# Kernel optimization log

Measured on AMD Instinct MI355X. Metric: run time of the kernel, lower is better.

The kernel has to match this reference:

```python
import jax, jax.numpy as jnp
import numpy as np

ATT = 256  # att_fc_size
MIN_W = 32  # min_width_feat
EPS = 1e-5  # InstanceNorm eps


def setup_inputs() -> dict:
    key = jax.random.key(0)
    ks = jax.random.split(key, 16)
    B, C, H, W = 32, 256, 128, 256
    hid = 256
    s = 0.02
    inp = {
        'features': jax.random.normal(ks[0], (B, C, H, W), jnp.float32),
        'prev_attn_weights': jax.random.uniform(ks[1], (B, H), jnp.float32),
        'coverage_vector': jax.random.uniform(ks[2], (B, H), jnp.float32) * 2.0,
        'hidden_h': jax.random.normal(ks[3], (1, B, hid), jnp.float32),
        # dense_width: Linear(min_width, 1)
        'w_width': jax.random.normal(ks[4], (MIN_W, 1), jnp.float32) * s,
        'b_width': jnp.zeros((1,), jnp.float32),
        # dense_enc: Linear(C, att)
        'w_enc': jax.random.normal(ks[5], (C, ATT), jnp.float32) * s,
        'b_enc': jnp.zeros((ATT,), jnp.float32),
        # conv_block: Conv1d(2, 16, k=15, pad=7)  (OIW layout)
        'conv_w': jax.random.normal(ks[6], (16, 2, 15), jnp.float32) * s,
        'conv_b': jnp.zeros((16,), jnp.float32),
        # dense_conv_block: Linear(16, att)
        'w_cb': jax.random.normal(ks[7], (16, ATT), jnp.float32) * s,
        'b_cb': jnp.zeros((ATT,), jnp.float32),
        # dense_hidden: Linear(hidden, att)
        'w_hid': jax.random.normal(ks[8], (hid, ATT), jnp.float32) * s,
        'b_hid': jnp.zeros((ATT,), jnp.float32),
        # dense_align: Linear(att, 1)
        'w_align': jax.random.normal(ks[9], (ATT, 1), jnp.float32) * s,
        'b_align': jnp.zeros((1,), jnp.float32),
    }
    return inp


def reference(features, prev_attn_weights, coverage_vector, hidden_h,
              w_width, b_width, w_enc, b_enc, conv_w, conv_b,
              w_cb, b_cb, w_hid, b_hid, w_align, b_align):
    B, C, H, W = features.shape
    # AdaptiveMaxPool2d((None, MIN_W)) with W % MIN_W == 0 -> uniform window max
    hf = features.reshape(B, C, H, MIN_W, W // MIN_W).max(axis=-1)  # (B,C,H,MIN_W)
    # dense_width -> (B,C,H)
    h_features = (jnp.einsum('bchm,mo->bcho', hf, w_width) + b_width)[..., 0]
    # branch 1: dense_enc on (B,H,C)
    s = jnp.einsum('bhc,ca->bha', h_features.transpose(0, 2, 1), w_enc) + b_enc
    # location + coverage channels: (B,2,H)
    cat = jnp.stack([prev_attn_weights, jnp.clip(coverage_vector, 0.0, 1.0)], axis=1)
    # InstanceNorm1d (no affine): per (b, channel) over H
    mu = cat.mean(axis=-1, keepdims=True)
    var = cat.var(axis=-1, keepdims=True)
    cat = (cat - mu) * jax.lax.rsqrt(var + EPS)
    # Conv1d(2 -> 16, k=15, pad=7)
    conv = jax.lax.conv_general_dilated(
        cat, conv_w, window_strides=(1,), padding=[(7, 7)],
        dimension_numbers=('NCH', 'OIH', 'NCH')) + conv_b[None, :, None]  # (B,16,H)
    s = s + jnp.einsum('bhk,ka->bha', conv.transpose(0, 2, 1), w_cb) + b_cb
    # hidden branch: (1,B,hid) -> (1,B,att) -> (B,1,att), broadcasts over H
    hsum = (jnp.einsum('lbd,da->lba', hidden_h, w_hid) + b_hid).transpose(1, 0, 2)
    s = s + hsum
    s = jnp.tanh(s)
    align_score = jnp.einsum('bha,ao->bho', s, w_align) + b_align  # (B,H,1)
    attn = jax.nn.softmax(align_score, axis=1)  # softmax over H
    # context: features^T(H<->W) @ attn -> (B,C,W)
    context = jnp.einsum('bchw,bh->bcw', features, attn[..., 0])
    return context, attn[..., 0]
```

## Files before the change

### kernel.cpp

```cpp
#include <hip/hip_runtime.h>
#include <hip/hip_bf16.h>

#define B_DIM 32
#define C_DIM 256
#define H_DIM 128
#define W_DIM 256
#define ATT_DIM 256

__global__ __launch_bounds__(256) void ka_fused(
    const float* __restrict__ feat, const float* __restrict__ w_width,
    const float* __restrict__ b_width,
    const float* __restrict__ prev, const float* __restrict__ cov,
    const float* __restrict__ conv_w, const float* __restrict__ conv_b,
    const float* __restrict__ hidden, const float* __restrict__ w_hid,
    const float* __restrict__ b_hid, const float* __restrict__ b_enc,
    const float* __restrict__ b_cb,
    float* __restrict__ hf, float* __restrict__ convT, float* __restrict__ hsum)
{
  const int tid = threadIdx.x;
  const int bid = blockIdx.x;

  if (bid < 8192) {
    __shared__ float res[H_DIM];
    const int lane = tid & 63, wid = tid >> 6;
    const float wv = w_width[lane >> 1] * 0.5f;
    const float bw = b_width[0];
    const float* base = feat + (size_t)bid * H_DIM * W_DIM + lane * 4;
#pragma unroll 4
    for (int i = 0; i < 32; i++) {
      const int h = wid + 4 * i;
      float4 v4 = *reinterpret_cast<const float4*>(base + (size_t)h * W_DIM);
      float v = fmaxf(fmaxf(v4.x, v4.y), fmaxf(v4.z, v4.w));
      v = fmaxf(v, __shfl_xor(v, 1));
      float contrib = v * wv;
#pragma unroll
      for (int off = 32; off >= 1; off >>= 1) contrib += __shfl_xor(contrib, off);
      if (lane == 0) res[h] = contrib + bw;
    }
    __syncthreads();
    if (tid < H_DIM)
      hf[(size_t)bid * H_DIM + tid] = res[tid];
  } else if (bid < 8224) {
    const int b = bid - 8192;
    __shared__ float n0[H_DIM], n1[H_DIM];
    __shared__ float ws4[2][4];
    __shared__ float cw[480];
    for (int i = tid; i < 480; i += 256) cw[i] = conv_w[i];
    const int lane = tid & 63, wv2 = tid >> 6;
    float x0 = 0.f, x1 = 0.f;
    if (tid < 128) {
      x0 = prev[b * H_DIM + tid];
      x1 = cov[b * H_DIM + tid];
      x1 = fminf(fmaxf(x1, 0.0f), 1.0f);
      float s0 = x0, q0 = x0 * x0, s1 = x1, q1 = x1 * x1;
#pragma unroll
      for (int off = 32; off >= 1; off >>= 1) {
        s0 += __shfl_xor(s0, off); q0 += __shfl_xor(q0, off);
        s1 += __shfl_xor(s1, off); q1 += __shfl_xor(q1, off);
      }
      if (lane == 0) { ws4[wv2][0] = s0; ws4[wv2][1] = q0; ws4[wv2][2] = s1; ws4[wv2][3] = q1; }
    }
    __syncthreads();
    if (tid < 128) {
      float S0 = ws4[0][0] + ws4[1][0], Q0 = ws4[0][1] + ws4[1][1];
      float S1 = ws4[0][2] + ws4[1][2], Q1 = ws4[0][3] + ws4[1][3];
      const float rH = 1.0f / H_DIM;
      float mu0 = S0 * rH, mu1 = S1 * rH;
      float inv0 = 1.0f / sqrtf(Q0 * rH - mu0 * mu0 + 1e-5f);
      float inv1 = 1.0f / sqrtf(Q1 * rH - mu1 * mu1 + 1e-5f);
      n0[tid] = (x0 - mu0) * inv0;
      n1[tid] = (x1 - mu1) * inv1;
    }
    __syncthreads();
    if (tid < 128) {
      float o[16];
#pragma unroll
      for (int k = 0; k < 16; k++) o[k] = conv_b[k];
#pragma unroll
      for (int j = 0; j < 15; j++) {
        int hh = tid - 7 + j;
        if (hh >= 0 && hh < H_DIM) {
          float f0 = n0[hh], f1 = n1[hh];
#pragma unroll
          for (int k = 0; k < 16; k++)
            o[k] += f0 * cw[k * 30 + j] + f1 * cw[k * 30 + 15 + j];
        }
      }
      float* outp = convT + ((size_t)(b * H_DIM + tid)) * 16;
#pragma unroll
      for (int k = 0; k < 16; k++) outp[k] = o[k];
    }
  } else {
    const int b = bid - 8224;
    const int a = tid;
    float acc = b_hid[a] + b_enc[a] + b_cb[a];
    const float* hb = hidden + b * 256;
#pragma unroll 4
    for (int d = 0; d < 256; d++) acc += hb[d] * w_hid[d * ATT_DIM + a];
    hsum[b * ATT_DIM + a] = acc;
  }
}

__global__ __launch_bounds__(256) void kb_gemm_align(
    const float* __restrict__ hf, const float* __restrict__ convT,
    const float* __restrict__ hsum, const float* __restrict__ w_enc,
    const float* __restrict__ w_cb, const float* __restrict__ w_align,
    const float* __restrict__ b_align, float* __restrict__ align_out)
{
  __shared__ float At[C_DIM][12];
  __shared__ float Ct[16][9];
  __shared__ float red[8][ATT_DIM];
  const int tid = threadIdx.x;
  const int m0 = blockIdx.x * 8;
  const int b = m0 >> 7;
  const int h0 = m0 & 127;
  const float* hp = hf + ((size_t)(b * C_DIM + tid)) * H_DIM + h0;
  float4 r0 = *reinterpret_cast<const float4*>(hp);
  float4 r1 = *reinterpret_cast<const float4*>(hp + 4);
  *reinterpret_cast<float4*>(&At[tid][0]) = r0;
  *reinterpret_cast<float4*>(&At[tid][4]) = r1;
  if (tid < 128) {
    int m = tid >> 4, k = tid & 15;
    Ct[k][m] = convT[(size_t)(b * H_DIM + h0) * 16 + tid];
  }
  __syncthreads();
  float acc[8];
#pragma unroll
  for (int m = 0; m < 8; m++) acc[m] = 0.0f;
  const float* wep = w_enc + tid;
#pragma unroll 4
  for (int k = 0; k < C_DIM; k++) {
    float bv = wep[k * ATT_DIM];
    const float4 a0 = *reinterpret_cast<const float4*>(&At[k][0]);
    const float4 a1 = *reinterpret_cast<const float4*>(&At[k][4]);
    acc[0] += a0.x * bv; acc[1] += a0.y * bv; acc[2] += a0.z * bv; acc[3] += a0.w * bv;
    acc[4] += a1.x * bv; acc[5] += a1.y * bv; acc[6] += a1.z * bv; acc[7] += a1.w * bv;
  }
#pragma unroll
  for (int k = 0; k < 16; k++) {
    float bv = w_cb[k * ATT_DIM + tid];
#pragma unroll
    for (int m = 0; m < 8; m++) acc[m] += Ct[k][m] * bv;
  }
  const float hs = hsum[b * ATT_DIM + tid];
  const float wa = w_align[tid];
#pragma unroll
  for (int m = 0; m < 8; m++)
    red[m][tid] = tanhf(acc[m] + hs) * wa;
  __syncthreads();
  const int lane = tid & 63, wid = tid >> 6;
  const float ba = b_align[0];
  for (int m = wid; m < 8; m += 4) {
    float s = red[m][lane] + red[m][lane + 64] + red[m][lane + 128] + red[m][lane + 192];
#pragma unroll
    for (int off = 32; off >= 1; off >>= 1) s += __shfl_xor(s, off);
    if (lane == 0) align_out[m0 + m] = s + ba;
  }
}

__global__ __launch_bounds__(256) void kc_context(
    const float* __restrict__ feat, const float* __restrict__ align,
    float* __restrict__ attn_out, float* __restrict__ ctx)
{
  const int bc = 8191 - blockIdx.x;
  const int b = bc >> 8, c = bc & 255;
  const int tid = threadIdx.x;
  __shared__ float al[H_DIM], at[H_DIM];
  if (tid < H_DIM) al[tid] = align[(b << 7) + tid];
  __syncthreads();
  if (tid < 64) {
    float a0 = al[tid], a1 = al[tid + 64];
    float mx = fmaxf(a0, a1);
#pragma unroll
    for (int off = 32; off >= 1; off >>= 1) mx = fmaxf(mx, __shfl_xor(mx, off));
    float e0 = expf(a0 - mx), e1 = expf(a1 - mx);
    float s = e0 + e1;
#pragma unroll
    for (int off = 32; off >= 1; off >>= 1) s += __shfl_xor(s, off);
    float inv = 1.0f / s;
    at[tid] = e0 * inv;
    at[tid + 64] = e1 * inv;
  }
  __syncthreads();
  if (c == 0 && tid < H_DIM) attn_out[(b << 7) + tid] = at[tid];
  const int g = tid >> 6, lane = tid & 63;
  const float* base = feat + (size_t)bc * H_DIM * W_DIM + lane * 4;
  float4 acc = make_float4(0.f, 0.f, 0.f, 0.f);
#pragma unroll 4
  for (int h = g; h < H_DIM; h += 4) {
    float4 v = *reinterpret_cast<const float4*>(base + (size_t)h * W_DIM);
    float a = at[h];
    acc.x += v.x * a; acc.y += v.y * a; acc.z += v.z * a; acc.w += v.w * a;
  }
  __shared__ float4 part[4][64];
  part[g][lane] = acc;
  __syncthreads();
  if (tid < 64) {
    float4 r0 = part[0][tid], r1 = part[1][tid], r2 = part[2][tid], r3 = part[3][tid];
    float4 o;
    o.x = r0.x + r1.x + r2.x + r3.x;
    o.y = r0.y + r1.y + r2.y + r3.y;
    o.z = r0.z + r1.z + r2.z + r3.z;
    o.w = r0.w + r1.w + r2.w + r3.w;
    *reinterpret_cast<float4*>(ctx + (size_t)bc * W_DIM + tid * 4) = o;
  }
}

extern "C" void kernel_launch(void* const* d_in, const int* in_sizes, int n_in,
                              void* d_out, int out_size, void* d_ws, size_t ws_size,
                              hipStream_t stream)
{
  const float* feat    = (const float*)d_in[0];
  const float* prev    = (const float*)d_in[1];
  const float* cov     = (const float*)d_in[2];
  const float* hidden  = (const float*)d_in[3];
  const float* w_width = (const float*)d_in[4];
  const float* b_width = (const float*)d_in[5];
  const float* w_enc   = (const float*)d_in[6];
  const float* b_enc   = (const float*)d_in[7];
  const float* conv_w  = (const float*)d_in[8];
  const float* conv_b  = (const float*)d_in[9];
  const float* w_cb    = (const float*)d_in[10];
  const float* b_cb    = (const float*)d_in[11];
  const float* w_hid   = (const float*)d_in[12];
  const float* b_hid   = (const float*)d_in[13];
  const float* w_align = (const float*)d_in[14];
  const float* b_align = (const float*)d_in[15];

  float* ctx_out  = (float*)d_out;
  float* attn_out = (float*)d_out + (size_t)B_DIM * C_DIM * W_DIM;

  float* ws    = (float*)d_ws;
  float* hf    = ws;
  float* convT = hf + 1048576;
  float* hsum  = convT + 65536;
  float* align = hsum + 8192;

  ka_fused<<<dim3(8192 + 32 + 32), dim3(256), 0, stream>>>(
      feat, w_width, b_width, prev, cov, conv_w, conv_b,
      hidden, w_hid, b_hid, b_enc, b_cb, hf, convT, hsum);
  kb_gemm_align<<<dim3((B_DIM * H_DIM) / 8), dim3(256), 0, stream>>>(
      hf, convT, hsum, w_enc, w_cb, w_align, b_align, align);
  kc_context<<<dim3(B_DIM * C_DIM), dim3(256), 0, stream>>>(
      feat, align, attn_out, ctx_out);
}
```

Measured before the change: 400.6 us.

## Split pipeline into batch chunks so features stay cache-resident between passes

Runs the pool, GEMM/align and context kernels per chunk of 8 batches instead of over the whole batch at once. The goal is for the second read of the features in the context pass to hit the last-level cache, which the first pass just filled, rather than HBM. In exchange it launches four times as many kernels and adds serialization between small grids; the mid-stage GEMM kernel now runs only 128 blocks.

```diff
diff --git a/kernel.cpp b/kernel.cpp
--- a/kernel.cpp
+++ b/kernel.cpp
@@ -6,8 +6,10 @@
 #define H_DIM 128
 #define W_DIM 256
 #define ATT_DIM 256
-
-__global__ __launch_bounds__(256) void ka_fused(
+#define G_CHUNK 8
+#define N_CHUNK (B_DIM / G_CHUNK)
+
+__global__ __launch_bounds__(256) void ka_chunk(
     const float* __restrict__ feat, const float* __restrict__ w_width,
     const float* __restrict__ b_width,
     const float* __restrict__ prev, const float* __restrict__ cov,
@@ -15,17 +17,20 @@
     const float* __restrict__ hidden, const float* __restrict__ w_hid,
     const float* __restrict__ b_hid, const float* __restrict__ b_enc,
     const float* __restrict__ b_cb,
-    float* __restrict__ hf, float* __restrict__ convT, float* __restrict__ hsum)
+    float* __restrict__ hf, float* __restrict__ convT, float* __restrict__ hsum,
+    int b0)
 {
   const int tid = threadIdx.x;
   const int bid = blockIdx.x;
-
-  if (bid < 8192) {
+  const int NPOOL = G_CHUNK * C_DIM;
+
+  if (bid < NPOOL) {
     __shared__ float res[H_DIM];
     const int lane = tid & 63, wid = tid >> 6;
+    const int bc = b0 * C_DIM + bid;
     const float wv = w_width[lane >> 1] * 0.5f;
     const float bw = b_width[0];
-    const float* base = feat + (size_t)bid * H_DIM * W_DIM + lane * 4;
+    const float* base = feat + (size_t)bc * H_DIM * W_DIM + lane * 4;
 #pragma unroll 4
     for (int i = 0; i < 32; i++) {
       const int h = wid + 4 * i;
@@ -39,9 +44,9 @@
     }
     __syncthreads();
     if (tid < H_DIM)
-      hf[(size_t)bid * H_DIM + tid] = res[tid];
-  } else if (bid < 8224) {
-    const int b = bid - 8192;
+      hf[(size_t)bc * H_DIM + tid] = res[tid];
+  } else if (bid < NPOOL + G_CHUNK) {
+    const int b = b0 + (bid - NPOOL);
     __shared__ float n0[H_DIM], n1[H_DIM];
     __shared__ float ws4[2][4];
     __shared__ float cw[480];
@@ -91,7 +96,7 @@
       for (int k = 0; k < 16; k++) outp[k] = o[k];
     }
   } else {
-    const int b = bid - 8224;
+    const int b = b0 + (bid - NPOOL - G_CHUNK);
     const int a = tid;
     float acc = b_hid[a] + b_enc[a] + b_cb[a];
     const float* hb = hidden + b * 256;
@@ -101,17 +106,17 @@
   }
 }
 
-__global__ __launch_bounds__(256) void kb_gemm_align(
+__global__ __launch_bounds__(256) void kb_chunk(
     const float* __restrict__ hf, const float* __restrict__ convT,
     const float* __restrict__ hsum, const float* __restrict__ w_enc,
     const float* __restrict__ w_cb, const float* __restrict__ w_align,
-    const float* __restrict__ b_align, float* __restrict__ align_out)
+    const float* __restrict__ b_align, float* __restrict__ align_out, int b0)
 {
   __shared__ float At[C_DIM][12];
   __shared__ float Ct[16][9];
   __shared__ float red[8][ATT_DIM];
   const int tid = threadIdx.x;
-  const int m0 = blockIdx.x * 8;
+  const int m0 = b0 * H_DIM + blockIdx.x * 8;
   const int b = m0 >> 7;
   const int h0 = m0 & 127;
   const float* hp = hf + ((size_t)(b * C_DIM + tid)) * H_DIM + h0;
@@ -158,11 +163,11 @@
   }
 }
 
-__global__ __launch_bounds__(256) void kc_context(
+__global__ __launch_bounds__(256) void kc_chunk(
     const float* __restrict__ feat, const float* __restrict__ align,
-    float* __restrict__ attn_out, float* __restrict__ ctx)
-{
-  const int bc = 8191 - blockIdx.x;
+    float* __restrict__ attn_out, float* __restrict__ ctx, int b0)
+{
+  const int bc = b0 * C_DIM + (G_CHUNK * C_DIM - 1 - blockIdx.x);
   const int b = bc >> 8, c = bc & 255;
   const int tid = threadIdx.x;
   __shared__ float al[H_DIM], at[H_DIM];
@@ -236,11 +241,14 @@
   float* hsum  = convT + 65536;
   float* align = hsum + 8192;
 
-  ka_fused<<<dim3(8192 + 32 + 32), dim3(256), 0, stream>>>(
-      feat, w_width, b_width, prev, cov, conv_w, conv_b,
-      hidden, w_hid, b_hid, b_enc, b_cb, hf, convT, hsum);
-  kb_gemm_align<<<dim3((B_DIM * H_DIM) / 8), dim3(256), 0, stream>>>(
-      hf, convT, hsum, w_enc, w_cb, w_align, b_align, align);
-  kc_context<<<dim3(B_DIM * C_DIM), dim3(256), 0, stream>>>(
-      feat, align, attn_out, ctx_out);
-}
+  for (int g = 0; g < N_CHUNK; ++g) {
+    const int b0 = g * G_CHUNK;
+    ka_chunk<<<dim3(G_CHUNK * C_DIM + 2 * G_CHUNK), dim3(256), 0, stream>>>(
+        feat, w_width, b_width, prev, cov, conv_w, conv_b,
+        hidden, w_hid, b_hid, b_enc, b_cb, hf, convT, hsum, b0);
+    kb_chunk<<<dim3(G_CHUNK * H_DIM / 8), dim3(256), 0, stream>>>(
+        hf, convT, hsum, w_enc, w_cb, w_align, b_align, align, b0);
+    kc_chunk<<<dim3(G_CHUNK * C_DIM), dim3(256), 0, stream>>>(
+        feat, align, attn_out, ctx_out, b0);
+  }
+}
```

Result: slower. 565.0 us (+41.0%).
